# Kernel optimization log

Hardware: AMD Instinct MI355X
Metric: run time of the kernel (lower is better)

The kernel has to match this reference:

```python
import jax, jax.numpy as jnp
import numpy as np

H = 64  # rnn_size == input_size
CANVAS = 25


def _init_params(key, vocab_size):
    ks = jax.random.split(key, 14)
    s = 0.05
    p = {}
    p['embed'] = jax.random.normal(ks[0], (vocab_size + 1, H), jnp.float32) * s
    p['W_ih'] = jax.random.normal(ks[1], (4 * H, H), jnp.float32) * s
    p['W_hh'] = jax.random.normal(ks[2], (4 * H, H), jnp.float32) * s
    p['b_ih'] = jax.random.normal(ks[3], (4 * H,), jnp.float32) * s
    p['b_hh'] = jax.random.normal(ks[4], (4 * H,), jnp.float32) * s
    p['Wc'] = jax.random.normal(ks[5], (3, H), jnp.float32) * s
    p['bc'] = jax.random.normal(ks[6], (3,), jnp.float32) * s
    p['Ws'] = jax.random.normal(ks[7], (3, H), jnp.float32) * s
    p['bs'] = jax.random.normal(ks[8], (3,), jnp.float32) * s
    p['Wo'] = jax.random.normal(ks[9], (2, H), jnp.float32) * s
    p['bo'] = jax.random.normal(ks[10], (2,), jnp.float32) * s
    p['Wr1'] = jax.random.normal(ks[11], (32, H + 1 + 4), jnp.float32) * s
    p['br1'] = jnp.zeros((32,), jnp.float32)
    p['Wr2'] = jax.random.normal(ks[12], (1, 32), jnp.float32) * s
    p['br2'] = jnp.zeros((1,), jnp.float32)
    return p


def setup_inputs() -> dict:
    key = jax.random.key(0)
    k1, k2, k3, k4, k5 = jax.random.split(key, 5)
    B, T, V = 4096, 128, 32000
    inp = {
        'inst': jax.random.randint(k1, (B, T), 0, V, dtype=jnp.int64)
        if jax.config.jax_enable_x64 else jax.random.randint(k1, (B, T), 0, V, dtype=jnp.int32),
        'prev_canvas': jax.random.normal(k2, (B, CANVAS, 4), jnp.float32),
        'ref_obj': jax.random.normal(k3, (B, 4), jnp.float32),
        'target_obj': jax.random.normal(k4, (B, 4), jnp.float32),
    }
    inp.update(_init_params(k5, V))
    return inp


def _encode(inst, embed, W_ih, W_hh, b_ih, b_hh):
    # inst: [B, T] -> h: [B, H] via sequential LSTMCell
    xs = embed[inst]                       # [B, T, H]
    xs = jnp.swapaxes(xs, 0, 1)            # [T, B, H]
    B = inst.shape[0]
    h0 = jnp.zeros((B, H), xs.dtype)
    c0 = jnp.zeros((B, H), xs.dtype)

    def step(carry, x):
        h, c = carry
        gates = x @ W_ih.T + b_ih + h @ W_hh.T + b_hh   # [B, 4H]
        i, f, g, o = jnp.split(gates, 4, axis=-1)
        i, f, o = jax.nn.sigmoid(i), jax.nn.sigmoid(f), jax.nn.sigmoid(o)
        c = f * c + i * jnp.tanh(g)
        h = o * jnp.tanh(c)
        return (h, c), None

    (h, _), _ = jax.lax.scan(step, (h0, c0), xs)
    return h


def _act_tag(inst):
    # 1.0 if last token with value >= 1 equals 9, else 0.0
    T = inst.shape[1]
    mask = inst >= 1                                   # [B, T]
    last_pos = T - 1 - jnp.argmax(mask[:, ::-1], axis=1)
    last_val = jnp.take_along_axis(inst, last_pos[:, None], axis=1)[:, 0]
    tag = jnp.where((last_val == 9) & mask.any(axis=1), 1.0, 0.0)
    return tag.astype(jnp.float32)


def reference(inst, prev_canvas, ref_obj, target_obj, embed, W_ih, W_hh, b_ih, b_hh,
              Wc, bc, Ws, bs, Wo, bo, Wr1, br1, Wr2, br2):
    h = _encode(inst, embed, W_ih, W_hh, b_ih, b_hh)           # [B, H]
    tag = _act_tag(inst)                                       # [B]
    inst2 = jnp.concatenate([h, tag[:, None]], axis=1)         # [B, H+1]
    inst2 = jnp.broadcast_to(inst2[:, None, :], (h.shape[0], CANVAS, H + 1))
    feat = jnp.concatenate([inst2, prev_canvas], axis=2)       # [B, 25, 69]
    hid = jax.nn.relu(jnp.einsum('bnf,of->bno', feat, Wr1) + br1)
    score = (jnp.einsum('bno,ro->bnr', hid, Wr2) + br2)[..., 0]  # [B, 25]
    weight = jax.nn.softmax(score, axis=1)
    ref_pred = jnp.einsum('bn,bnd->bd', weight, prev_canvas)   # [B, 4]
    offset = jnp.clip(h @ Wo.T + bo, -1.0, 1.0)                # hardtanh, [B, 2]
    color_out = jax.nn.log_softmax(h @ Wc.T + bc, axis=1)      # [B, 3]
    shape_out = jax.nn.log_softmax(h @ Ws.T + bs, axis=1)      # [B, 3]
    row_out = ref_pred[:, 2] + offset[:, 0]
    col_out = ref_pred[:, 3] + offset[:, 1]
    return (color_out, shape_out, row_out, col_out)
```

## Files before the change

### kernel.cpp

```cpp
#include <hip/hip_runtime.h>
#include <hip/hip_bf16.h>

#define HH 64
#define TT 128
#define TP 132
#define BT 4
#define NVOC 32001

typedef __attribute__((ext_vector_type(8))) short bf16x8;
typedef __attribute__((ext_vector_type(4))) float f32x4;

__device__ __forceinline__ unsigned short f2bf(float f) {
  union { float f; unsigned u; } v; v.f = f;
  return (unsigned short)((v.u + 0x8000u) >> 16);
}
__device__ __forceinline__ float bfh(unsigned short u) {
  union { float f; unsigned u; } v; v.u = ((unsigned)u) << 16; return v.f;
}
__device__ __forceinline__ float rcp_(float x) { return __builtin_amdgcn_rcpf(x); }

__device__ __forceinline__ float sighalf(float y) {
  const float yc = fminf(0.85f, fmaxf(-0.85f, y));
  const float t = yc * yc;
  return fmaf(yc, fmaf(t, fmaf(t, 0.06666667f, -0.16666667f), 0.5f), 0.5f);
}
__device__ __forceinline__ float ptanh(float y) {
  const float t = y * y;
  const float num = y * fmaf(t, 105.f + t, 945.f);
  const float den = fmaf(t, fmaf(t, 15.f, 420.f), 945.f);
  return num * rcp_(den);
}
__device__ __forceinline__ float red32(float v) {
#pragma unroll
  for (int s = 16; s; s >>= 1) v += __shfl_xor(v, s, 32);
  return v;
}

#define MFMA(acc, a, b) acc = __builtin_amdgcn_mfma_f32_16x16x32_bf16(a, b, acc, 0, 0, 0)

__global__ __launch_bounds__(256) void xproj_k(
    const float* __restrict__ embed, const float* __restrict__ Wih,
    const float* __restrict__ bih, const float* __restrict__ bhh,
    unsigned short* __restrict__ xp)
{
  const int tid = threadIdx.x, lane = tid & 63, w = tid >> 6;
  const int fr = lane & 15, fg = lane >> 4;
  const int mt = blockIdx.x * 4 + w;
  if (mt >= 2001) return;
  const int tb = mt * 16;
  int ta = tb + fr; if (ta > NVOC - 1) ta = NVOC - 1;
  const float* ea = embed + (size_t)ta * 64 + fg * 8;
  bf16x8 a0, a1;
#pragma unroll
  for (int j = 0; j < 8; j++) { a0[j] = (short)f2bf(ea[j]); a1[j] = (short)f2bf(ea[32 + j]); }
  const f32x4 z4 = {0.f, 0.f, 0.f, 0.f};
  for (int nt = 0; nt < 16; nt++) {
    const int n = nt * 16 + fr;
    const int q = n & 3, jj = n >> 2;
    const int grow = q * 64 + jj;
    const float* wp = Wih + (size_t)grow * 64 + fg * 8;
    bf16x8 b0, b1;
#pragma unroll
    for (int j = 0; j < 8; j++) { b0[j] = (short)f2bf(wp[j]); b1[j] = (short)f2bf(wp[32 + j]); }
    f32x4 D = z4;
    MFMA(D, a0, b0); MFMA(D, a1, b1);
    const float bias = bih[grow] + bhh[grow];
    const float scale = (q == 2) ? 1.f : 0.5f;
#pragma unroll
    for (int r = 0; r < 4; r++) {
      const int tk = tb + fg * 4 + r;
      if (tk < NVOC) xp[(size_t)tk * 256 + n] = f2bf(scale * (D[r] + bias));
    }
  }
}

__global__ __launch_bounds__(256, 4) void lstm_k(
    const int* __restrict__ inst, const unsigned short* __restrict__ xp,
    const float* __restrict__ Whh,
    const float* __restrict__ canvas,
    const float* __restrict__ Wc, const float* __restrict__ bc,
    const float* __restrict__ Ws, const float* __restrict__ bs,
    const float* __restrict__ Wo, const float* __restrict__ bo,
    const float* __restrict__ Wr1, const float* __restrict__ br1,
    const float* __restrict__ Wr2, const float* __restrict__ br2,
    float* __restrict__ out, int B)
{
  __shared__ int tokT[BT * TP];
  __shared__ unsigned short hsh[2 * BT * HH];
  __shared__ float h_s[BT][68];
  __shared__ float Wr1_s[32 * 69];
  __shared__ float cv_s[BT * 100];

  const int tid  = threadIdx.x;
  const int lane = tid & 63;
  const int w    = tid >> 6;
  const int fr   = lane & 15;
  const int fg   = lane >> 4;
  const int b0   = blockIdx.x * BT;
  const int jcol = w * 16 + fr;
  const int rr   = fr >> 2;

  for (int i = tid; i < BT * TT; i += 256) {
    const int b = i >> 7, t = i & (TT - 1);
    tokT[b * TP + t] = inst[(size_t)(b0 + b) * TT + t];
  }
  for (int i = tid; i < 2 * BT * HH; i += 256) hsh[i] = 0;
  for (int i = tid; i < 32 * 69; i += 256) Wr1_s[i] = Wr1[i];
  for (int i = tid; i < BT * 100; i += 256) cv_s[i] = canvas[(size_t)b0 * 100 + i];

  bf16x8 whh[4][2];
#pragma unroll
  for (int q = 0; q < 4; q++) {
    const float scale = (q == 2) ? 1.f : 0.5f;
#pragma unroll
    for (int kt = 0; kt < 2; kt++) {
      const float* pb = Whh + (size_t)(q * 64 + jcol) * 64 + kt * 32 + fg * 8;
      bf16x8 fb;
#pragma unroll
      for (int j = 0; j < 8; j++) fb[j] = (short)f2bf(scale * pb[j]);
      whh[q][kt] = fb;
    }
  }

  const int ra = (rr * 128 + (fg * 16)) ^ (rr << 4);
  const int rb = (rr * 128 + 64 + (fg * 16)) ^ (rr << 4);
  const int wa = (fg * 128 + 2 * jcol) ^ (fg << 4);
  char* const hs0 = (char*)hsh;
  char* const hs1 = hs0 + BT * HH * 2;
  const int* const tokrow = tokT + fg * TP;
  const int jc4 = jcol << 2;

  __syncthreads();

  ushort4 xpA = *(const ushort4*)(xp + (size_t)tokrow[0] * 256 + jc4);
  ushort4 xpB = *(const ushort4*)(xp + (size_t)tokrow[1] * 256 + jc4);

  float cst = 0.f, hk = 0.f;
  const f32x4 z4 = {0.f, 0.f, 0.f, 0.f};

#define LSTM_STEP(XPC, RD, WR, T)                                              \
  {                                                                            \
    const ushort4 cur = XPC;                                                   \
    bf16x8 ha0 = *(const bf16x8*)((RD) + ra);                                  \
    bf16x8 ha1 = *(const bf16x8*)((RD) + rb);                                  \
    const int tn = ((T) + 2 < TT) ? (T) + 2 : TT - 1;                          \
    const int kk = tokrow[tn];                                                 \
    f32x4 D0 = z4, D1 = z4, D2 = z4, D3 = z4;                                  \
    MFMA(D0, ha0, whh[0][0]); MFMA(D1, ha0, whh[1][0]);                        \
    MFMA(D2, ha0, whh[2][0]); MFMA(D3, ha0, whh[3][0]);                        \
    MFMA(D0, ha1, whh[0][1]); MFMA(D1, ha1, whh[1][1]);                        \
    MFMA(D2, ha1, whh[2][1]); MFMA(D3, ha1, whh[3][1]);                        \
    XPC = *(const ushort4*)(xp + (size_t)kk * 256 + jc4);                      \
    const float si = sighalf(D0[0] + bfh(cur.x));                              \
    const float sf = sighalf(D1[0] + bfh(cur.y));                              \
    const float tg = ptanh(D2[0] + bfh(cur.z));                                \
    const float so = sighalf(D3[0] + bfh(cur.w));                              \
    const float c  = fmaf(sf, cst, si * tg);                                   \
    cst = c;                                                                   \
    hk = so * ptanh(c);                                                        \
    union { float f; unsigned u; } cv; cv.f = hk;                              \
    *(unsigned short*)((WR) + wa) = (unsigned short)((cv.u + 0x8000u) >> 16);  \
    asm volatile("s_waitcnt lgkmcnt(0)" ::: "memory");                         \
    __builtin_amdgcn_s_barrier();                                              \
  }

  for (int t = 0; t < TT; t += 2) {
    LSTM_STEP(xpA, hs0, hs1, t);
    LSTM_STEP(xpB, hs1, hs0, t + 1);
  }
#undef LSTM_STEP

  h_s[fg][jcol] = hk;
  __syncthreads();

  if (tid < 128) {
    const int m  = tid >> 5;
    const int o  = tid & 31;
    const int gb = b0 + m;

    int key = -1;
#pragma unroll
    for (int q = 0; q < 4; q++) {
      const int t = o + q * 32;
      const int tk = tokT[m * TP + t];
      if (tk >= 1) key = max(key, (t << 16) | tk);
    }
#pragma unroll
    for (int s = 16; s; s >>= 1) key = max(key, __shfl_xor(key, s, 32));
    const float tag = (key >= 0 && (key & 0xFFFF) == 9) ? 1.f : 0.f;

    float base = br1[o] + Wr1_s[o * 69 + 64] * tag;
    for (int f = 0; f < 64; f++) base += Wr1_s[o * 69 + f] * h_s[m][f];
    const float wr2o = Wr2[o];
    const float* cv = cv_s + m * 100;

    float sc[25];
    float mx = -1e30f;
#pragma unroll
    for (int n = 0; n < 25; n++) {
      float acc = base;
#pragma unroll
      for (int d = 0; d < 4; d++) acc += Wr1_s[o * 69 + 65 + d] * cv[n * 4 + d];
      float pp = wr2o * fmaxf(acc, 0.f);
#pragma unroll
      for (int s = 16; s; s >>= 1) pp += __shfl_xor(pp, s, 32);
      sc[n] = pp + br2[0];
      mx = fmaxf(mx, sc[n]);
    }
    float sum = 0.f, rp2 = 0.f, rp3 = 0.f;
#pragma unroll
    for (int n = 0; n < 25; n++) {
      const float e = __expf(sc[n] - mx);
      sum += e;
      rp2 += e * cv[n * 4 + 2];
      rp3 += e * cv[n * 4 + 3];
    }
    const float inv = 1.f / sum;

    const float h0 = h_s[m][o], h1 = h_s[m][o + 32];
    float c0 = red32(h0 * Wc[o]       + h1 * Wc[32 + o])  + bc[0];
    float c1 = red32(h0 * Wc[64 + o]  + h1 * Wc[96 + o])  + bc[1];
    float c2 = red32(h0 * Wc[128 + o] + h1 * Wc[160 + o]) + bc[2];
    float s0 = red32(h0 * Ws[o]       + h1 * Ws[32 + o])  + bs[0];
    float s1 = red32(h0 * Ws[64 + o]  + h1 * Ws[96 + o])  + bs[1];
    float s2 = red32(h0 * Ws[128 + o] + h1 * Ws[160 + o]) + bs[2];
    float o0 = red32(h0 * Wo[o]       + h1 * Wo[32 + o])  + bo[0];
    float o1 = red32(h0 * Wo[64 + o]  + h1 * Wo[96 + o])  + bo[1];
    o0 = fminf(fmaxf(o0, -1.f), 1.f);
    o1 = fminf(fmaxf(o1, -1.f), 1.f);

    const float cm = fmaxf(c0, fmaxf(c1, c2));
    const float cl = cm + __logf(__expf(c0 - cm) + __expf(c1 - cm) + __expf(c2 - cm));
    const float sm = fmaxf(s0, fmaxf(s1, s2));
    const float sl = sm + __logf(__expf(s0 - sm) + __expf(s1 - sm) + __expf(s2 - sm));

    if (o == 0) {
      out[gb * 3 + 0] = c0 - cl; out[gb * 3 + 1] = c1 - cl; out[gb * 3 + 2] = c2 - cl;
      float* shp = out + (size_t)3 * B;
      shp[gb * 3 + 0] = s0 - sl; shp[gb * 3 + 1] = s1 - sl; shp[gb * 3 + 2] = s2 - sl;
      out[(size_t)6 * B + gb] = rp2 * inv + o0;
      out[(size_t)7 * B + gb] = rp3 * inv + o1;
    }
  }
}

extern "C" void kernel_launch(void* const* d_in, const int* in_sizes, int n_in,
                              void* d_out, int out_size, void* d_ws, size_t ws_size,
                              hipStream_t stream) {
  const int*   inst   = (const int*)  d_in[0];
  const float* canvas = (const float*)d_in[1];
  const float* embed  = (const float*)d_in[4];
  const float* Wih    = (const float*)d_in[5];
  const float* Whh    = (const float*)d_in[6];
  const float* bih    = (const float*)d_in[7];
  const float* bhh    = (const float*)d_in[8];
  const float* Wc     = (const float*)d_in[9];
  const float* bc     = (const float*)d_in[10];
  const float* Ws_    = (const float*)d_in[11];
  const float* bs     = (const float*)d_in[12];
  const float* Wo     = (const float*)d_in[13];
  const float* bo     = (const float*)d_in[14];
  const float* Wr1    = (const float*)d_in[15];
  const float* br1    = (const float*)d_in[16];
  const float* Wr2    = (const float*)d_in[17];
  const float* br2    = (const float*)d_in[18];

  const int B = in_sizes[0] / TT;

  unsigned short* xp = (unsigned short*)d_ws;

  xproj_k<<<501, 256, 0, stream>>>(embed, Wih, bih, bhh, xp);
  lstm_k<<<B / BT, 256, 0, stream>>>(inst, xp, Whh,
                                     canvas, Wc, bc, Ws_, bs, Wo, bo,
                                     Wr1, br1, Wr2, br2, (float*)d_out, B);
}
```

Before: 120.6 us.

## Run each LSTM batch tile in a single wave to drop block barriers

The recurrent kernel now uses one 64-thread wave per block of 4 sequences instead of four waves. That wave computes all 16 gate tiles with 32 MFMAs per step and evaluates the gate nonlinearities for all 4 rows per lane. This removes the per-step workgroup barrier, and token indices are pre-shifted into byte offsets for the gate-table gather. In exchange, each SIMD holds far fewer waves to hide MFMA and gather latency, and each lane does 4x the elementwise work, partly spent on choosing among 16 accumulators.

```diff
diff --git a/kernel.cpp b/kernel.cpp
--- a/kernel.cpp
+++ b/kernel.cpp
@@ -3,7 +3,7 @@
 
 #define HH 64
 #define TT 128
-#define TP 132
+#define TOP 136
 #define BT 4
 #define NVOC 32001
 
@@ -36,7 +36,8 @@
   return v;
 }
 
-#define MFMA(acc, a, b) acc = __builtin_amdgcn_mfma_f32_16x16x32_bf16(a, b, acc, 0, 0, 0)
+#define MFMA_Z(a, b)    __builtin_amdgcn_mfma_f32_16x16x32_bf16(a, b, z4, 0, 0, 0)
+#define MFMA_A(a, b, c) __builtin_amdgcn_mfma_f32_16x16x32_bf16(a, b, c, 0, 0, 0)
 
 __global__ __launch_bounds__(256) void xproj_k(
     const float* __restrict__ embed, const float* __restrict__ Wih,
@@ -62,8 +63,8 @@
     bf16x8 b0, b1;
 #pragma unroll
     for (int j = 0; j < 8; j++) { b0[j] = (short)f2bf(wp[j]); b1[j] = (short)f2bf(wp[32 + j]); }
-    f32x4 D = z4;
-    MFMA(D, a0, b0); MFMA(D, a1, b1);
+    f32x4 D = MFMA_Z(a0, b0);
+    D = MFMA_A(a1, b1, D);
     const float bias = bih[grow] + bhh[grow];
     const float scale = (q == 2) ? 1.f : 0.5f;
 #pragma unroll
@@ -74,7 +75,7 @@
   }
 }
 
-__global__ __launch_bounds__(256, 4) void lstm_k(
+__global__ __launch_bounds__(64, 1) void lstm_k(
     const int* __restrict__ inst, const unsigned short* __restrict__ xp,
     const float* __restrict__ Whh,
     const float* __restrict__ canvas,
@@ -85,96 +86,113 @@
     const float* __restrict__ Wr2, const float* __restrict__ br2,
     float* __restrict__ out, int B)
 {
-  __shared__ int tokT[BT * TP];
-  __shared__ unsigned short hsh[2 * BT * HH];
+  __shared__ int toff[BT][TOP];
+  __shared__ unsigned short hsh[2][BT * HH];
   __shared__ float h_s[BT][68];
   __shared__ float Wr1_s[32 * 69];
   __shared__ float cv_s[BT * 100];
 
-  const int tid  = threadIdx.x;
-  const int lane = tid & 63;
-  const int w    = tid >> 6;
-  const int fr   = lane & 15;
-  const int fg   = lane >> 4;
-  const int b0   = blockIdx.x * BT;
-  const int jcol = w * 16 + fr;
-  const int rr   = fr >> 2;
-
-  for (int i = tid; i < BT * TT; i += 256) {
+  const int tid = threadIdx.x;
+  const int fr = tid & 15, fg = tid >> 4;
+  const int b0 = blockIdx.x * BT;
+  const int j0 = fg * 16 + fr;
+
+  for (int i = tid; i < BT * TT; i += 64) {
     const int b = i >> 7, t = i & (TT - 1);
-    tokT[b * TP + t] = inst[(size_t)(b0 + b) * TT + t];
-  }
-  for (int i = tid; i < 2 * BT * HH; i += 256) hsh[i] = 0;
-  for (int i = tid; i < 32 * 69; i += 256) Wr1_s[i] = Wr1[i];
-  for (int i = tid; i < BT * 100; i += 256) cv_s[i] = canvas[(size_t)b0 * 100 + i];
-
-  bf16x8 whh[4][2];
-#pragma unroll
-  for (int q = 0; q < 4; q++) {
+    toff[b][t] = inst[(size_t)(b0 + b) * TT + t] << 9;
+  }
+  for (int i = tid; i < 2 * BT * HH; i += 64) ((unsigned short*)hsh)[i] = 0;
+  for (int i = tid; i < 32 * 69; i += 64) Wr1_s[i] = Wr1[i];
+  for (int i = tid; i < BT * 100; i += 64) cv_s[i] = canvas[(size_t)b0 * 100 + i];
+
+  bf16x8 whh[16][2];
+#pragma unroll
+  for (int T = 0; T < 16; T++) {
+    const int q = T >> 2, k = T & 3;
+    const int n = q * 64 + k * 16 + fr;
     const float scale = (q == 2) ? 1.f : 0.5f;
 #pragma unroll
     for (int kt = 0; kt < 2; kt++) {
-      const float* pb = Whh + (size_t)(q * 64 + jcol) * 64 + kt * 32 + fg * 8;
-      bf16x8 fb;
-#pragma unroll
-      for (int j = 0; j < 8; j++) fb[j] = (short)f2bf(scale * pb[j]);
-      whh[q][kt] = fb;
-    }
-  }
-
-  const int ra = (rr * 128 + (fg * 16)) ^ (rr << 4);
-  const int rb = (rr * 128 + 64 + (fg * 16)) ^ (rr << 4);
-  const int wa = (fg * 128 + 2 * jcol) ^ (fg << 4);
-  char* const hs0 = (char*)hsh;
-  char* const hs1 = hs0 + BT * HH * 2;
-  const int* const tokrow = tokT + fg * TP;
-  const int jc4 = jcol << 2;
+      const float* p = Whh + (size_t)n * 64 + kt * 32 + fg * 8;
+      bf16x8 f;
+#pragma unroll
+      for (int j = 0; j < 8; j++) f[j] = (short)f2bf(scale * p[j]);
+      whh[T][kt] = f;
+    }
+  }
+
+  const int rrow = fr & 3;
+  const int ra = (rrow * 128 + fg * 16) ^ (rrow << 4);
+  const int rb = (rrow * 128 + 64 + fg * 16) ^ (rrow << 4);
+  int wwa[4];
+#pragma unroll
+  for (int r = 0; r < 4; r++) wwa[r] = (r * 128 + j0 * 2) ^ (r << 4);
+  char* const hb0 = (char*)&hsh[0][0];
+  char* const hb1 = (char*)&hsh[1][0];
 
   __syncthreads();
 
-  ushort4 xpA = *(const ushort4*)(xp + (size_t)tokrow[0] * 256 + jc4);
-  ushort4 xpB = *(const ushort4*)(xp + (size_t)tokrow[1] * 256 + jc4);
-
-  float cst = 0.f, hk = 0.f;
+  const char* const xpb = (const char*)xp;
+  const int j8 = j0 * 8;
+
+  ushort4 xgA[4], xgB[4];
+#pragma unroll
+  for (int r = 0; r < 4; r++) xgA[r] = *(const ushort4*)(xpb + toff[r][0] + j8);
+#pragma unroll
+  for (int r = 0; r < 4; r++) xgB[r] = *(const ushort4*)(xpb + toff[r][1] + j8);
+
+  float cst[4] = {0.f, 0.f, 0.f, 0.f};
+  float hk[4];
   const f32x4 z4 = {0.f, 0.f, 0.f, 0.f};
-
-#define LSTM_STEP(XPC, RD, WR, T)                                              \
+  const bool fb0 = (fg & 1) != 0, fb1 = (fg & 2) != 0;
+
+#define STEP(XG, RD, WR, T)                                                    \
   {                                                                            \
-    const ushort4 cur = XPC;                                                   \
     bf16x8 ha0 = *(const bf16x8*)((RD) + ra);                                  \
     bf16x8 ha1 = *(const bf16x8*)((RD) + rb);                                  \
     const int tn = ((T) + 2 < TT) ? (T) + 2 : TT - 1;                          \
-    const int kk = tokrow[tn];                                                 \
-    f32x4 D0 = z4, D1 = z4, D2 = z4, D3 = z4;                                  \
-    MFMA(D0, ha0, whh[0][0]); MFMA(D1, ha0, whh[1][0]);                        \
-    MFMA(D2, ha0, whh[2][0]); MFMA(D3, ha0, whh[3][0]);                        \
-    MFMA(D0, ha1, whh[0][1]); MFMA(D1, ha1, whh[1][1]);                        \
-    MFMA(D2, ha1, whh[2][1]); MFMA(D3, ha1, whh[3][1]);                        \
-    XPC = *(const ushort4*)(xp + (size_t)kk * 256 + jc4);                      \
-    const float si = sighalf(D0[0] + bfh(cur.x));                              \
-    const float sf = sighalf(D1[0] + bfh(cur.y));                              \
-    const float tg = ptanh(D2[0] + bfh(cur.z));                                \
-    const float so = sighalf(D3[0] + bfh(cur.w));                              \
-    const float c  = fmaf(sf, cst, si * tg);                                   \
-    cst = c;                                                                   \
-    hk = so * ptanh(c);                                                        \
-    union { float f; unsigned u; } cv; cv.f = hk;                              \
-    *(unsigned short*)((WR) + wa) = (unsigned short)((cv.u + 0x8000u) >> 16);  \
-    asm volatile("s_waitcnt lgkmcnt(0)" ::: "memory");                         \
-    __builtin_amdgcn_s_barrier();                                              \
+    const ushort4 nx0 = *(const ushort4*)(xpb + toff[0][tn] + j8);             \
+    const ushort4 nx1 = *(const ushort4*)(xpb + toff[1][tn] + j8);             \
+    const ushort4 nx2 = *(const ushort4*)(xpb + toff[2][tn] + j8);             \
+    const ushort4 nx3 = *(const ushort4*)(xpb + toff[3][tn] + j8);             \
+    f32x4 D[16];                                                               \
+    _Pragma("unroll")                                                          \
+    for (int T2 = 0; T2 < 16; T2++) {                                          \
+      D[T2] = MFMA_Z(ha0, whh[T2][0]);                                         \
+      D[T2] = MFMA_A(ha1, whh[T2][1], D[T2]);                                  \
+    }                                                                          \
+    _Pragma("unroll")                                                          \
+    for (int r = 0; r < 4; r++) {                                              \
+      const float g0 = fb1 ? (fb0 ? D[3][r]  : D[2][r])  : (fb0 ? D[1][r]  : D[0][r]);  \
+      const float g1 = fb1 ? (fb0 ? D[7][r]  : D[6][r])  : (fb0 ? D[5][r]  : D[4][r]);  \
+      const float g2 = fb1 ? (fb0 ? D[11][r] : D[10][r]) : (fb0 ? D[9][r]  : D[8][r]);  \
+      const float g3 = fb1 ? (fb0 ? D[15][r] : D[14][r]) : (fb0 ? D[13][r] : D[12][r]); \
+      const float si = sighalf(g0 + bfh(XG[r].x));                             \
+      const float sf = sighalf(g1 + bfh(XG[r].y));                             \
+      const float tg = ptanh (g2 + bfh(XG[r].z));                              \
+      const float so = sighalf(g3 + bfh(XG[r].w));                             \
+      const float c  = fmaf(sf, cst[r], si * tg);                              \
+      cst[r] = c;                                                              \
+      const float hn = so * ptanh(c);                                          \
+      hk[r] = hn;                                                              \
+      union { float f; unsigned u; } cv; cv.f = hn;                            \
+      *(unsigned short*)((WR) + wwa[r]) = (unsigned short)((cv.u + 0x8000u) >> 16); \
+    }                                                                          \
+    XG[0] = nx0; XG[1] = nx1; XG[2] = nx2; XG[3] = nx3;                        \
   }
 
   for (int t = 0; t < TT; t += 2) {
-    LSTM_STEP(xpA, hs0, hs1, t);
-    LSTM_STEP(xpB, hs1, hs0, t + 1);
-  }
-#undef LSTM_STEP
-
-  h_s[fg][jcol] = hk;
+    STEP(xgA, hb0, hb1, t);
+    STEP(xgB, hb1, hb0, t + 1);
+  }
+#undef STEP
+
+#pragma unroll
+  for (int r = 0; r < 4; r++) h_s[r][j0] = hk[r];
   __syncthreads();
 
-  if (tid < 128) {
-    const int m  = tid >> 5;
+  for (int p = 0; p < 2; p++) {
+    const int m  = p * 2 + (tid >> 5);
     const int o  = tid & 31;
     const int gb = b0 + m;
 
@@ -182,7 +200,7 @@
 #pragma unroll
     for (int q = 0; q < 4; q++) {
       const int t = o + q * 32;
-      const int tk = tokT[m * TP + t];
+      const int tk = toff[m][t] >> 9;
       if (tk >= 1) key = max(key, (t << 16) | tk);
     }
 #pragma unroll
@@ -270,7 +288,7 @@
   unsigned short* xp = (unsigned short*)d_ws;
 
   xproj_k<<<501, 256, 0, stream>>>(embed, Wih, bih, bhh, xp);
-  lstm_k<<<B / BT, 256, 0, stream>>>(inst, xp, Whh,
-                                     canvas, Wc, bc, Ws_, bs, Wo, bo,
-                                     Wr1, br1, Wr2, br2, (float*)d_out, B);
-}
+  lstm_k<<<B / BT, 64, 0, stream>>>(inst, xp, Whh,
+                                    canvas, Wc, bc, Ws_, bs, Wo, bo,
+                                    Wr1, br1, Wr2, br2, (float*)d_out, B);
+}
```

Result: slower. 149.3 us (+23.7%).
